# Kernel optimization log

Measured on AMD Instinct MI355X. Metric: run time of the kernel, lower is better.

Reference implementation:

```python
import jax, jax.numpy as jnp
import numpy as np
from jax import lax

EPS = 1e-06
S = 0.025
ALPHA = 0.98
DELTA = 2.0
R = 0.5


def setup_inputs() -> dict:
    key = jax.random.key(0)
    # magnitude spectrogram: [batch, freq, time], nonnegative
    x = jax.random.uniform(key, (32, 256, 4096), dtype=jnp.float32)
    return {"x": x}


def reference(x):
    # x: [B, F, T]; EMA smoother runs over the time axis (last dim).
    # m_0 = s*x_0 ; m_t = (1-s)*m_{t-1} + s*x_t  (init carry 0 reproduces m_0 = s*x_0)
    xt = jnp.moveaxis(x, 2, 0)  # [T, B, F]

    def step(m, frame):
        m = (1.0 - S) * m + S * frame
        return m, m

    _, M = lax.scan(step, jnp.zeros_like(xt[0]), xt)  # [T, B, F]
    M = jnp.moveaxis(M, 0, 2)  # [B, F, T]
    # power-law compression fused elementwise
    return (x / (M + EPS) ** ALPHA + DELTA) ** R - DELTA ** R
```

## Files before the change

kernel.cpp:

```cpp
#include <hip/hip_runtime.h>


constexpr int T_LEN   = 4096;
constexpr int LANES   = 64;
constexpr int SUBS    = 4;
constexpr int TILE    = LANES * 4 * SUBS;
constexpr int TILE_F4 = TILE / 4;
constexpr int NTILE   = T_LEN / TILE;
constexpr int WAVES_PER_BLK = 4;
constexpr int NTHR    = LANES * WAVES_PER_BLK;

constexpr float EPSF = 1e-6f;
constexpr float SF   = 0.025f;
constexpr float A1F  = 0.975f;

constexpr double dA1   = 0.975;
constexpr double dA2   = dA1 * dA1;
constexpr double dA4   = dA2 * dA2;
constexpr double dA8   = dA4 * dA4;
constexpr double dA16  = dA8 * dA8;
constexpr double dA32  = dA16 * dA16;
constexpr double dA64  = dA32 * dA32;
constexpr double dA128 = dA64 * dA64;
constexpr double dA256 = dA128 * dA128;

__global__ __launch_bounds__(NTHR, 8) void pcen_wave_kernel(
    const float* __restrict__ x, float* __restrict__ out, int rows)
{
    const int lane = threadIdx.x & 63;
    const int wave = threadIdx.x >> 6;
    const int row  = blockIdx.x * WAVES_PER_BLK + wave;
    if (row >= rows) return;

    const long long base = (long long)row * T_LEN;
    const float4* __restrict__ px   = (const float4*)(x + base);
    float4* __restrict__       pout = (float4*)(out + base);

    const float cA4   = (float)dA4;
    const float cA8   = (float)dA8;
    const float cA16  = (float)dA16;
    const float cA32  = (float)dA32;
    const float cA64  = (float)dA64;
    const float cA128 = (float)dA128;
    const float cA256 = (float)dA256;

    float flane = 1.0f;
    if (lane & 1)  flane *= cA4;
    if (lane & 2)  flane *= cA8;
    if (lane & 4)  flane *= cA16;
    if (lane & 8)  flane *= cA32;
    if (lane & 16) flane *= cA64;
    if (lane & 32) flane *= cA128;

    const float SQRT_D = 1.41421356237309515f;

    float4 buf[SUBS];
#pragma unroll
    for (int j = 0; j < SUBS; ++j) buf[j] = px[j * LANES + lane];

    float carry = 0.0f;

#pragma unroll
    for (int t = 0; t < NTILE; ++t) {
        float4 nxt[SUBS];
        if (t < NTILE - 1) {
#pragma unroll
            for (int j = 0; j < SUBS; ++j)
                nxt[j] = px[(t + 1) * TILE_F4 + j * LANES + lane];
        }

        float Sv[SUBS];
#pragma unroll
        for (int j = 0; j < SUBS; ++j) {
            float m = SF * buf[j].x;
            m = fmaf(A1F, m, SF * buf[j].y);
            m = fmaf(A1F, m, SF * buf[j].z);
            m = fmaf(A1F, m, SF * buf[j].w);
            Sv[j] = m;
        }

#pragma unroll
        for (int j = 0; j < SUBS; ++j) {
            float tt;
            tt = __shfl_up(Sv[j], 1,  64); if (lane >= 1)  Sv[j] = fmaf(cA4,   tt, Sv[j]);
            tt = __shfl_up(Sv[j], 2,  64); if (lane >= 2)  Sv[j] = fmaf(cA8,   tt, Sv[j]);
            tt = __shfl_up(Sv[j], 4,  64); if (lane >= 4)  Sv[j] = fmaf(cA16,  tt, Sv[j]);
            tt = __shfl_up(Sv[j], 8,  64); if (lane >= 8)  Sv[j] = fmaf(cA32,  tt, Sv[j]);
            tt = __shfl_up(Sv[j], 16, 64); if (lane >= 16) Sv[j] = fmaf(cA64,  tt, Sv[j]);
            tt = __shfl_up(Sv[j], 32, 64); if (lane >= 32) Sv[j] = fmaf(cA128, tt, Sv[j]);
        }

        float seed[SUBS];
#pragma unroll
        for (int j = 0; j < SUBS; ++j) {
            float excl = __shfl_up(Sv[j], 1, 64);
            if (lane == 0) excl = 0.0f;
            float last = __shfl(Sv[j], 63, 64);
            seed[j] = fmaf(flane, carry, excl);
            carry   = fmaf(cA256, carry, last);
        }

#pragma unroll
        for (int j = 0; j < SUBS; ++j) {
            float4 v = buf[j];
            float  m = seed[j];
            float4 o;
            m = fmaf(A1F, m, SF * v.x);
            o.x = __builtin_amdgcn_sqrtf(
                      fmaf(v.x, __builtin_amdgcn_exp2f(
                          -0.98f * __builtin_amdgcn_logf(m + EPSF)), 2.0f)) - SQRT_D;
            m = fmaf(A1F, m, SF * v.y);
            o.y = __builtin_amdgcn_sqrtf(
                      fmaf(v.y, __builtin_amdgcn_exp2f(
                          -0.98f * __builtin_amdgcn_logf(m + EPSF)), 2.0f)) - SQRT_D;
            m = fmaf(A1F, m, SF * v.z);
            o.z = __builtin_amdgcn_sqrtf(
                      fmaf(v.z, __builtin_amdgcn_exp2f(
                          -0.98f * __builtin_amdgcn_logf(m + EPSF)), 2.0f)) - SQRT_D;
            m = fmaf(A1F, m, SF * v.w);
            o.w = __builtin_amdgcn_sqrtf(
                      fmaf(v.w, __builtin_amdgcn_exp2f(
                          -0.98f * __builtin_amdgcn_logf(m + EPSF)), 2.0f)) - SQRT_D;
            pout[t * TILE_F4 + j * LANES + lane] = o;
        }

#pragma unroll
        for (int j = 0; j < SUBS; ++j) buf[j] = nxt[j];
    }
}

extern "C" void kernel_launch(void* const* d_in, const int* in_sizes, int n_in,
                              void* d_out, int out_size, void* d_ws, size_t ws_size,
                              hipStream_t stream) {
    const float* x = (const float*)d_in[0];
    float* out = (float*)d_out;
    const int rows = in_sizes[0] / T_LEN;
    const int blocks = (rows + WAVES_PER_BLK - 1) / WAVES_PER_BLK;
    pcen_wave_kernel<<<dim3(blocks), dim3(NTHR), 0, stream>>>(x, out, rows);
}
```

Baseline: 232.4 us.

## Load entire row into registers upfront, processing in two halves

Replaces the four-tile double-buffered loop with issuing all 16 float4 loads per lane at kernel start (two halves of 8), then scanning and writing each half. This puts more memory requests in flight per wave to hide latency, at the cost of many more VGPRs. The launch_bounds occupancy hint of 8 is dropped, so occupancy may fall.

```diff
diff --git a/kernel.cpp b/kernel.cpp
--- a/kernel.cpp
+++ b/kernel.cpp
@@ -1,14 +1,12 @@
 #include <hip/hip_runtime.h>
 
 
-constexpr int T_LEN   = 4096;
-constexpr int LANES   = 64;
-constexpr int SUBS    = 4;
-constexpr int TILE    = LANES * 4 * SUBS;
-constexpr int TILE_F4 = TILE / 4;
-constexpr int NTILE   = T_LEN / TILE;
+constexpr int T_LEN = 4096;
+constexpr int LANES = 64;
+constexpr int NSUB  = 16;
+constexpr int HALF  = 8;
 constexpr int WAVES_PER_BLK = 4;
-constexpr int NTHR    = LANES * WAVES_PER_BLK;
+constexpr int NTHR  = LANES * WAVES_PER_BLK;
 
 constexpr float EPSF = 1e-6f;
 constexpr float SF   = 0.025f;
@@ -24,7 +22,7 @@
 constexpr double dA128 = dA64 * dA64;
 constexpr double dA256 = dA128 * dA128;
 
-__global__ __launch_bounds__(NTHR, 8) void pcen_wave_kernel(
+__global__ __launch_bounds__(NTHR) void pcen_wave_kernel(
     const float* __restrict__ x, float* __restrict__ out, int rows)
 {
     const int lane = threadIdx.x & 63;
@@ -54,56 +52,45 @@
 
     const float SQRT_D = 1.41421356237309515f;
 
-    float4 buf[SUBS];
+    float4 dA_[HALF];
 #pragma unroll
-    for (int j = 0; j < SUBS; ++j) buf[j] = px[j * LANES + lane];
+    for (int s = 0; s < HALF; ++s) dA_[s] = px[s * LANES + lane];
+    float4 dB_[HALF];
+#pragma unroll
+    for (int s = 0; s < HALF; ++s) dB_[s] = px[(HALF + s) * LANES + lane];
 
     float carry = 0.0f;
 
+    {
+        float Sv[HALF];
 #pragma unroll
-    for (int t = 0; t < NTILE; ++t) {
-        float4 nxt[SUBS];
-        if (t < NTILE - 1) {
+        for (int s = 0; s < HALF; ++s) {
+            float m = SF * dA_[s].x;
+            m = fmaf(A1F, m, SF * dA_[s].y);
+            m = fmaf(A1F, m, SF * dA_[s].z);
+            m = fmaf(A1F, m, SF * dA_[s].w);
+            Sv[s] = m;
+        }
 #pragma unroll
-            for (int j = 0; j < SUBS; ++j)
-                nxt[j] = px[(t + 1) * TILE_F4 + j * LANES + lane];
+        for (int s = 0; s < HALF; ++s) {
+            float tt;
+            tt = __shfl_up(Sv[s], 1,  64); if (lane >= 1)  Sv[s] = fmaf(cA4,   tt, Sv[s]);
+            tt = __shfl_up(Sv[s], 2,  64); if (lane >= 2)  Sv[s] = fmaf(cA8,   tt, Sv[s]);
+            tt = __shfl_up(Sv[s], 4,  64); if (lane >= 4)  Sv[s] = fmaf(cA16,  tt, Sv[s]);
+            tt = __shfl_up(Sv[s], 8,  64); if (lane >= 8)  Sv[s] = fmaf(cA32,  tt, Sv[s]);
+            tt = __shfl_up(Sv[s], 16, 64); if (lane >= 16) Sv[s] = fmaf(cA64,  tt, Sv[s]);
+            tt = __shfl_up(Sv[s], 32, 64); if (lane >= 32) Sv[s] = fmaf(cA128, tt, Sv[s]);
         }
+#pragma unroll
+        for (int s = 0; s < HALF; ++s) {
+            float excl = __shfl_up(Sv[s], 1, 64);
+            if (lane == 0) excl = 0.0f;
+            float last = __shfl(Sv[s], 63, 64);
 
-        float Sv[SUBS];
-#pragma unroll
-        for (int j = 0; j < SUBS; ++j) {
-            float m = SF * buf[j].x;
-            m = fmaf(A1F, m, SF * buf[j].y);
-            m = fmaf(A1F, m, SF * buf[j].z);
-            m = fmaf(A1F, m, SF * buf[j].w);
-            Sv[j] = m;
-        }
+            float m = fmaf(flane, carry, excl);
+            carry   = fmaf(cA256, carry, last);
 
-#pragma unroll
-        for (int j = 0; j < SUBS; ++j) {
-            float tt;
-            tt = __shfl_up(Sv[j], 1,  64); if (lane >= 1)  Sv[j] = fmaf(cA4,   tt, Sv[j]);
-            tt = __shfl_up(Sv[j], 2,  64); if (lane >= 2)  Sv[j] = fmaf(cA8,   tt, Sv[j]);
-            tt = __shfl_up(Sv[j], 4,  64); if (lane >= 4)  Sv[j] = fmaf(cA16,  tt, Sv[j]);
-            tt = __shfl_up(Sv[j], 8,  64); if (lane >= 8)  Sv[j] = fmaf(cA32,  tt, Sv[j]);
-            tt = __shfl_up(Sv[j], 16, 64); if (lane >= 16) Sv[j] = fmaf(cA64,  tt, Sv[j]);
-            tt = __shfl_up(Sv[j], 32, 64); if (lane >= 32) Sv[j] = fmaf(cA128, tt, Sv[j]);
-        }
-
-        float seed[SUBS];
-#pragma unroll
-        for (int j = 0; j < SUBS; ++j) {
-            float excl = __shfl_up(Sv[j], 1, 64);
-            if (lane == 0) excl = 0.0f;
-            float last = __shfl(Sv[j], 63, 64);
-            seed[j] = fmaf(flane, carry, excl);
-            carry   = fmaf(cA256, carry, last);
-        }
-
-#pragma unroll
-        for (int j = 0; j < SUBS; ++j) {
-            float4 v = buf[j];
-            float  m = seed[j];
+            float4 v = dA_[s];
             float4 o;
             m = fmaf(A1F, m, SF * v.x);
             o.x = __builtin_amdgcn_sqrtf(
@@ -121,11 +108,61 @@
             o.w = __builtin_amdgcn_sqrtf(
                       fmaf(v.w, __builtin_amdgcn_exp2f(
                           -0.98f * __builtin_amdgcn_logf(m + EPSF)), 2.0f)) - SQRT_D;
-            pout[t * TILE_F4 + j * LANES + lane] = o;
+
+            pout[s * LANES + lane] = o;
         }
+    }
 
+    {
+        float Sv[HALF];
 #pragma unroll
-        for (int j = 0; j < SUBS; ++j) buf[j] = nxt[j];
+        for (int s = 0; s < HALF; ++s) {
+            float m = SF * dB_[s].x;
+            m = fmaf(A1F, m, SF * dB_[s].y);
+            m = fmaf(A1F, m, SF * dB_[s].z);
+            m = fmaf(A1F, m, SF * dB_[s].w);
+            Sv[s] = m;
+        }
+#pragma unroll
+        for (int s = 0; s < HALF; ++s) {
+            float tt;
+            tt = __shfl_up(Sv[s], 1,  64); if (lane >= 1)  Sv[s] = fmaf(cA4,   tt, Sv[s]);
+            tt = __shfl_up(Sv[s], 2,  64); if (lane >= 2)  Sv[s] = fmaf(cA8,   tt, Sv[s]);
+            tt = __shfl_up(Sv[s], 4,  64); if (lane >= 4)  Sv[s] = fmaf(cA16,  tt, Sv[s]);
+            tt = __shfl_up(Sv[s], 8,  64); if (lane >= 8)  Sv[s] = fmaf(cA32,  tt, Sv[s]);
+            tt = __shfl_up(Sv[s], 16, 64); if (lane >= 16) Sv[s] = fmaf(cA64,  tt, Sv[s]);
+            tt = __shfl_up(Sv[s], 32, 64); if (lane >= 32) Sv[s] = fmaf(cA128, tt, Sv[s]);
+        }
+#pragma unroll
+        for (int s = 0; s < HALF; ++s) {
+            float excl = __shfl_up(Sv[s], 1, 64);
+            if (lane == 0) excl = 0.0f;
+            float last = __shfl(Sv[s], 63, 64);
+
+            float m = fmaf(flane, carry, excl);
+            carry   = fmaf(cA256, carry, last);
+
+            float4 v = dB_[s];
+            float4 o;
+            m = fmaf(A1F, m, SF * v.x);
+            o.x = __builtin_amdgcn_sqrtf(
+                      fmaf(v.x, __builtin_amdgcn_exp2f(
+                          -0.98f * __builtin_amdgcn_logf(m + EPSF)), 2.0f)) - SQRT_D;
+            m = fmaf(A1F, m, SF * v.y);
+            o.y = __builtin_amdgcn_sqrtf(
+                      fmaf(v.y, __builtin_amdgcn_exp2f(
+                          -0.98f * __builtin_amdgcn_logf(m + EPSF)), 2.0f)) - SQRT_D;
+            m = fmaf(A1F, m, SF * v.z);
+            o.z = __builtin_amdgcn_sqrtf(
+                      fmaf(v.z, __builtin_amdgcn_exp2f(
+                          -0.98f * __builtin_amdgcn_logf(m + EPSF)), 2.0f)) - SQRT_D;
+            m = fmaf(A1F, m, SF * v.w);
+            o.w = __builtin_amdgcn_sqrtf(
+                      fmaf(v.w, __builtin_amdgcn_exp2f(
+                          -0.98f * __builtin_amdgcn_logf(m + EPSF)), 2.0f)) - SQRT_D;
+
+            pout[(HALF + s) * LANES + lane] = o;
+        }
     }
 }
 
```

New measurement: 234.2 us. About the same (+0.8%).

## Load whole row into registers upfront instead of double-buffered tiles

Applied to the files above, without the earlier changes.

Replaces the tiled double-buffered loop with a single up-front load of all 16 float4 chunks of the row per lane, then runs the local scan, the wave-level shuffle scans and the output pass over the full row. The aim is to put every global load for the row in flight at once, exposing more memory-level parallelism than the one-tile-ahead prefetch. It also drops the occupancy hint of 8 from launch_bounds. The cost is much higher register use, which can lower occupancy for a memory-bound kernel.

```diff
diff --git a/kernel.cpp b/kernel.cpp
--- a/kernel.cpp
+++ b/kernel.cpp
@@ -1,14 +1,11 @@
 #include <hip/hip_runtime.h>
 
 
-constexpr int T_LEN   = 4096;
-constexpr int LANES   = 64;
-constexpr int SUBS    = 4;
-constexpr int TILE    = LANES * 4 * SUBS;
-constexpr int TILE_F4 = TILE / 4;
-constexpr int NTILE   = T_LEN / TILE;
+constexpr int T_LEN = 4096;
+constexpr int LANES = 64;
+constexpr int NSUB  = 16;
 constexpr int WAVES_PER_BLK = 4;
-constexpr int NTHR    = LANES * WAVES_PER_BLK;
+constexpr int NTHR  = LANES * WAVES_PER_BLK;
 
 constexpr float EPSF = 1e-6f;
 constexpr float SF   = 0.025f;
@@ -24,7 +21,7 @@
 constexpr double dA128 = dA64 * dA64;
 constexpr double dA256 = dA128 * dA128;
 
-__global__ __launch_bounds__(NTHR, 8) void pcen_wave_kernel(
+__global__ __launch_bounds__(NTHR) void pcen_wave_kernel(
     const float* __restrict__ x, float* __restrict__ out, int rows)
 {
     const int lane = threadIdx.x & 63;
@@ -54,78 +51,63 @@
 
     const float SQRT_D = 1.41421356237309515f;
 
-    float4 buf[SUBS];
+    float4 d[NSUB];
 #pragma unroll
-    for (int j = 0; j < SUBS; ++j) buf[j] = px[j * LANES + lane];
+    for (int s = 0; s < NSUB; ++s) d[s] = px[s * LANES + lane];
+
+    asm volatile("" ::: "memory");
+
+    float Sv[NSUB];
+#pragma unroll
+    for (int s = 0; s < NSUB; ++s) {
+        float m = SF * d[s].x;
+        m = fmaf(A1F, m, SF * d[s].y);
+        m = fmaf(A1F, m, SF * d[s].z);
+        m = fmaf(A1F, m, SF * d[s].w);
+        Sv[s] = m;
+    }
+
+#pragma unroll
+    for (int s = 0; s < NSUB; ++s) {
+        float tt;
+        tt = __shfl_up(Sv[s], 1,  64); if (lane >= 1)  Sv[s] = fmaf(cA4,   tt, Sv[s]);
+        tt = __shfl_up(Sv[s], 2,  64); if (lane >= 2)  Sv[s] = fmaf(cA8,   tt, Sv[s]);
+        tt = __shfl_up(Sv[s], 4,  64); if (lane >= 4)  Sv[s] = fmaf(cA16,  tt, Sv[s]);
+        tt = __shfl_up(Sv[s], 8,  64); if (lane >= 8)  Sv[s] = fmaf(cA32,  tt, Sv[s]);
+        tt = __shfl_up(Sv[s], 16, 64); if (lane >= 16) Sv[s] = fmaf(cA64,  tt, Sv[s]);
+        tt = __shfl_up(Sv[s], 32, 64); if (lane >= 32) Sv[s] = fmaf(cA128, tt, Sv[s]);
+    }
 
     float carry = 0.0f;
+#pragma unroll
+    for (int s = 0; s < NSUB; ++s) {
+        float excl = __shfl_up(Sv[s], 1, 64);
+        if (lane == 0) excl = 0.0f;
+        float last = __shfl(Sv[s], 63, 64);
 
-#pragma unroll
-    for (int t = 0; t < NTILE; ++t) {
-        float4 nxt[SUBS];
-        if (t < NTILE - 1) {
-#pragma unroll
-            for (int j = 0; j < SUBS; ++j)
-                nxt[j] = px[(t + 1) * TILE_F4 + j * LANES + lane];
-        }
+        float m = fmaf(flane, carry, excl);
+        carry   = fmaf(cA256, carry, last);
 
-        float Sv[SUBS];
-#pragma unroll
-        for (int j = 0; j < SUBS; ++j) {
-            float m = SF * buf[j].x;
-            m = fmaf(A1F, m, SF * buf[j].y);
-            m = fmaf(A1F, m, SF * buf[j].z);
-            m = fmaf(A1F, m, SF * buf[j].w);
-            Sv[j] = m;
-        }
+        float4 v = d[s];
+        float4 o;
+        m = fmaf(A1F, m, SF * v.x);
+        o.x = __builtin_amdgcn_sqrtf(
+                  fmaf(v.x, __builtin_amdgcn_exp2f(
+                      -0.98f * __builtin_amdgcn_logf(m + EPSF)), 2.0f)) - SQRT_D;
+        m = fmaf(A1F, m, SF * v.y);
+        o.y = __builtin_amdgcn_sqrtf(
+                  fmaf(v.y, __builtin_amdgcn_exp2f(
+                      -0.98f * __builtin_amdgcn_logf(m + EPSF)), 2.0f)) - SQRT_D;
+        m = fmaf(A1F, m, SF * v.z);
+        o.z = __builtin_amdgcn_sqrtf(
+                  fmaf(v.z, __builtin_amdgcn_exp2f(
+                      -0.98f * __builtin_amdgcn_logf(m + EPSF)), 2.0f)) - SQRT_D;
+        m = fmaf(A1F, m, SF * v.w);
+        o.w = __builtin_amdgcn_sqrtf(
+                  fmaf(v.w, __builtin_amdgcn_exp2f(
+                      -0.98f * __builtin_amdgcn_logf(m + EPSF)), 2.0f)) - SQRT_D;
 
-#pragma unroll
-        for (int j = 0; j < SUBS; ++j) {
-            float tt;
-            tt = __shfl_up(Sv[j], 1,  64); if (lane >= 1)  Sv[j] = fmaf(cA4,   tt, Sv[j]);
-            tt = __shfl_up(Sv[j], 2,  64); if (lane >= 2)  Sv[j] = fmaf(cA8,   tt, Sv[j]);
-            tt = __shfl_up(Sv[j], 4,  64); if (lane >= 4)  Sv[j] = fmaf(cA16,  tt, Sv[j]);
-            tt = __shfl_up(Sv[j], 8,  64); if (lane >= 8)  Sv[j] = fmaf(cA32,  tt, Sv[j]);
-            tt = __shfl_up(Sv[j], 16, 64); if (lane >= 16) Sv[j] = fmaf(cA64,  tt, Sv[j]);
-            tt = __shfl_up(Sv[j], 32, 64); if (lane >= 32) Sv[j] = fmaf(cA128, tt, Sv[j]);
-        }
-
-        float seed[SUBS];
-#pragma unroll
-        for (int j = 0; j < SUBS; ++j) {
-            float excl = __shfl_up(Sv[j], 1, 64);
-            if (lane == 0) excl = 0.0f;
-            float last = __shfl(Sv[j], 63, 64);
-            seed[j] = fmaf(flane, carry, excl);
-            carry   = fmaf(cA256, carry, last);
-        }
-
-#pragma unroll
-        for (int j = 0; j < SUBS; ++j) {
-            float4 v = buf[j];
-            float  m = seed[j];
-            float4 o;
-            m = fmaf(A1F, m, SF * v.x);
-            o.x = __builtin_amdgcn_sqrtf(
-                      fmaf(v.x, __builtin_amdgcn_exp2f(
-                          -0.98f * __builtin_amdgcn_logf(m + EPSF)), 2.0f)) - SQRT_D;
-            m = fmaf(A1F, m, SF * v.y);
-            o.y = __builtin_amdgcn_sqrtf(
-                      fmaf(v.y, __builtin_amdgcn_exp2f(
-                          -0.98f * __builtin_amdgcn_logf(m + EPSF)), 2.0f)) - SQRT_D;
-            m = fmaf(A1F, m, SF * v.z);
-            o.z = __builtin_amdgcn_sqrtf(
-                      fmaf(v.z, __builtin_amdgcn_exp2f(
-                          -0.98f * __builtin_amdgcn_logf(m + EPSF)), 2.0f)) - SQRT_D;
-            m = fmaf(A1F, m, SF * v.w);
-            o.w = __builtin_amdgcn_sqrtf(
-                      fmaf(v.w, __builtin_amdgcn_exp2f(
-                          -0.98f * __builtin_amdgcn_logf(m + EPSF)), 2.0f)) - SQRT_D;
-            pout[t * TILE_F4 + j * LANES + lane] = o;
-        }
-
-#pragma unroll
-        for (int j = 0; j < SUBS; ++j) buf[j] = nxt[j];
+        pout[s * LANES + lane] = o;
     }
 }
 
```

Measured after the change: 235.2 us. No clear change (+1.2%).
